# Kernel optimization log

Measured on AMD Instinct MI355X. Metric: run time of the kernel, lower is better.

The kernel has to match this reference:

```python
import jax, jax.numpy as jnp
import numpy as np

HID = 16  # comparator hidden channels, Conv1(2,16) -> Conv1(16,1)


def setup_inputs() -> dict:
    key = jax.random.key(0)
    k0, k1, k2 = jax.random.split(key, 3)
    B, N = 32, 512
    x = jax.random.normal(k0, (B, 1, N), dtype=jnp.float32)
    # xavier_uniform for 1x1 convs, zero bias (as in PermNet.__init__)
    g1 = (6.0 / (2 + HID)) ** 0.5
    g2 = (6.0 / (HID + 1)) ** 0.5
    w1 = jax.random.uniform(k1, (HID, 2), jnp.float32, -g1, g1)
    b1 = jnp.zeros((HID,), jnp.float32)
    w2 = jax.random.uniform(k2, (1, HID), jnp.float32, -g2, g2)
    b2 = jnp.zeros((1,), jnp.float32)
    lr = jnp.ones((1,), jnp.float32)  # learned step size, used via abs()
    return {"x": x, "w1": w1, "b1": b1, "w2": w2, "b2": b2, "lr": lr,
            "steps": 8, "temp": 1}


def reference(x, w1, b1, w2, b2, lr, steps, temp):
    B, C, N = x.shape  # C == 1 (scalar set elements)
    temp = jnp.asarray(temp, x.dtype)

    # --- Comparator: pairwise 1x1-conv MLP over all (i, j) pairs ---
    xi = jnp.broadcast_to(x[:, 0, :, None], (B, N, N))  # element i
    xj = jnp.broadcast_to(x[:, 0, None, :], (B, N, N))  # element j
    pairs = jnp.stack([xi, xj], axis=1)                  # (B, 2, N, N)
    h = jax.nn.relu(jnp.einsum('oc,bcij->boij', w1, pairs)
                    + b1[None, :, None, None])           # (B, HID, N, N)
    c = (jnp.einsum('oc,bcij->boij', w2, h)
         + b2[None, :, None, None])[:, 0]                # (B, N, N)
    c = c - jnp.swapaxes(c, -1, -2)  # antisymmetric ordering cost C(i,j)=-C(j,i)

    # --- calculate_assignment: iterative differentiable permutation ---
    # a[b, i, k] = weight of element i being placed at position k
    lr_abs = jnp.abs(lr)[0]
    a0 = jnp.full((B, N, N), 1.0 / N, dtype=x.dtype)

    def step(a, _):
        csum = jnp.cumsum(a, axis=-1)      # sum_{l<=k} a[., j, l]
        total = csum[..., -1:]
        left = csum - a                     # sum_{l<k}
        right = total - csum                # sum_{l>k}
        m = right - left                    # (B, N, N)
        # d(total cost)/d a_{ik} = sum_j C_{ij} * (right_{jk} - left_{jk})
        grad = jnp.einsum('bij,bjk->bik', c, m)
        a_new = jax.nn.softmax((a - lr_abs * grad) / temp, axis=-1)
        return a_new, None

    a, _ = jax.lax.scan(step, a0, None, length=steps)

    # --- apply_assignment: permute elements into positions ---
    y = jnp.einsum('bci,bik->bck', x, a)  # (B, 1, N)
    return y, a
```

## Files before the change

kernel.cpp:

```cpp
#include <hip/hip_runtime.h>
#include <hip/hip_bf16.h>
#include <math.h>

#define B_   32
#define N_   512
#define HID_ 16

typedef __attribute__((ext_vector_type(8))) short bf16x8;
typedef __attribute__((ext_vector_type(4))) float f32x4;

union U8 { ushort u[8]; uint4 v; };

__device__ __forceinline__ ushort f2bf(float f) {
    __hip_bfloat16 h = __float2bfloat16(f);
    return *reinterpret_cast<ushort*>(&h);
}
__device__ __forceinline__ float bf2f(ushort u) {
    return __uint_as_float(((unsigned int)u) << 16);
}

__device__ __forceinline__ void gload16(const void* g, void* l) {
    __builtin_amdgcn_global_load_lds(
        (const __attribute__((address_space(1))) unsigned int*)g,
        (__attribute__((address_space(3))) unsigned int*)l,
        16, 0, 0);
}

__device__ __forceinline__ int pidx(int r, int c) {
    return r * N_ + ((c + ((r >> 3) << 2)) & (N_ - 1));
}

__global__ __launch_bounds__(512)
void fused_kernel(const float* __restrict__ x,
                  const float* __restrict__ w1,
                  const float* __restrict__ b1,
                  const float* __restrict__ w2,
                  ushort* __restrict__ cB,
                  const ushort* __restrict__ aTin,
                  const ushort* __restrict__ aBin,
                  ushort* __restrict__ aTout,
                  ushort* __restrict__ aBout,
                  float* __restrict__ aout,
                  float* __restrict__ vg,
                  float* __restrict__ ypart,
                  const float* __restrict__ lr,
                  const int* __restrict__ temp,
                  int first, int last)
{
    __shared__ char smem[131072];
    __shared__ float sw1[2*HID_], sb1v[HID_], sw2v[HID_];
    float* Pl = (float*)smem;

    int iblk = blockIdx.x;
    int r8 = iblk & 7, m = iblk >> 3;
    int b  = r8 + ((m >> 3) << 3);
    int i0 = (m & 7) * 64;

    const size_t MATOFF = (size_t)b * N_ * N_;
    int tid = threadIdx.x, lane = tid & 63, w = tid >> 6;

    float lrv = fabsf(lr[0]);
    float ti  = 1.0f / (float)temp[0];
    float vrq[8];

    if (first) {
        if (tid < 2*HID_) sw1[tid] = w1[tid];
        if (tid < HID_)   { sb1v[tid] = b1[tid]; sw2v[tid] = w2[tid]; }
        __syncthreads();
        int k0 = lane * 8;
        float4 xj0 = *(const float4*)&x[b*N_ + k0];
        float4 xj1 = *(const float4*)&x[b*N_ + k0 + 4];
        float xjv[8] = {xj0.x, xj0.y, xj0.z, xj0.w, xj1.x, xj1.y, xj1.z, xj1.w};
        for (int q = 0; q < 8; ++q) {
            int grow = i0 + w*8 + q;
            float xi = x[b*N_ + grow];
            float s1[8] = {}, s2[8] = {};
            for (int o = 0; o < HID_; ++o) {
                float wa = sw1[2*o], wb = sw1[2*o+1], bo = sb1v[o], wo = sw2v[o];
                float Ao = fmaf(wa, xi, bo);
                float Co = fmaf(wb, xi, bo);
#pragma unroll
                for (int e = 0; e < 8; ++e) {
                    s1[e] = fmaf(wo, fmaxf(fmaf(wb, xjv[e], Ao), 0.f), s1[e]);
                    s2[e] = fmaf(wo, fmaxf(fmaf(wa, xjv[e], Co), 0.f), s2[e]);
                }
            }
            float rs = 0.f;
            U8 cb;
#pragma unroll
            for (int e = 0; e < 8; ++e) {
                float cv = s1[e] - s2[e];
                rs += cv;
                cb.u[e] = f2bf(cv);
            }
            *(uint4*)&cB[MATOFF + (size_t)grow * N_ + k0] = cb.v;
#pragma unroll
            for (int off = 1; off < 64; off <<= 1) rs += __shfl_xor(rs, off);
            vrq[q] = rs;
            if (lane == 0) vg[b*N_ + grow] = rs;
        }
    } else {
        const ushort* Ag = cB   + MATOFF + (size_t)i0 * N_;
        const ushort* Bg = aTin + MATOFF + (size_t)(w * 64) * N_;
        char* Asb = smem;
        char* Bw  = smem + 65536 + w * 8192;
        f32x4 acc[4][4] = {};

        {
            int r = tid >> 3, sl = tid & 7;
            const ushort* Asrc = Ag + (size_t)r * N_ + ((sl ^ (r & 7)) << 3);
#pragma unroll
            for (int c = 0; c < 8; ++c)
                gload16(Asrc + c*64, Asb + c*8192 + tid*16);
        }
        asm volatile("s_waitcnt vmcnt(0)" ::: "memory");
        __syncthreads();

        for (int kt = 0; kt < 8; ++kt) {
            asm volatile("s_waitcnt lgkmcnt(0)" ::: "memory");
#pragma unroll
            for (int g = 0; g < 8; ++g) {
                int r  = g*8 + (lane >> 3);
                int sl = lane & 7;
                gload16(Bg + (size_t)r * N_ + kt*64 + ((sl ^ (r & 7)) << 3),
                        Bw + g*1024 + lane*16);
            }
            asm volatile("s_waitcnt vmcnt(0)" ::: "memory");
            __builtin_amdgcn_sched_barrier(0);

#pragma unroll
            for (int kk = 0; kk < 2; ++kk) {
                bf16x8 af[4], bb[4];
#pragma unroll
                for (int f = 0; f < 4; ++f) {
                    int ra = f*16 + (lane & 15);
                    int sa = kk*4 + (lane >> 4);
                    af[f] = *(const bf16x8*)(Asb + kt*8192 + ra*128 + ((sa ^ (ra & 7)) << 4));
                    bb[f] = *(const bf16x8*)(Bw + ra*128 + ((sa ^ (ra & 7)) << 4));
                }
#pragma unroll
                for (int i = 0; i < 4; ++i)
#pragma unroll
                    for (int j = 0; j < 4; ++j)
                        acc[i][j] = __builtin_amdgcn_mfma_f32_16x16x32_bf16(
                                        af[i], bb[j], acc[i][j], 0, 0, 0);
            }
        }
        __syncthreads();

        {
            int h = lane >> 4, cl = lane & 15;
#pragma unroll
            for (int i = 0; i < 4; ++i)
#pragma unroll
                for (int j = 0; j < 4; ++j)
#pragma unroll
                    for (int r = 0; r < 4; ++r)
                        Pl[pidx(i*16 + h*4 + r, w*64 + j*16 + cl)] = acc[i][j][r];
        }
        __syncthreads();
    }

    float ysum[8] = {};

    for (int q = 0; q < 8; ++q) {
        int row  = w*8 + q;
        int grow = i0 + row;
        float vr = first ? vrq[q] : vg[b*N_ + grow];

        float pv[8], av[8];
        if (first) {
#pragma unroll
            for (int e = 0; e < 8; ++e) { pv[e] = vr * (1.0f/N_); av[e] = 1.0f/N_; }
        } else {
            int rot = (row >> 3) << 2;
            int c0  = (lane*8     + rot) & (N_-1);
            int c1  = (lane*8 + 4 + rot) & (N_-1);
            f32x4 p0 = *(const f32x4*)&Pl[row*N_ + c0];
            f32x4 p1 = *(const f32x4*)&Pl[row*N_ + c1];
            pv[0]=p0[0]; pv[1]=p0[1]; pv[2]=p0[2]; pv[3]=p0[3];
            pv[4]=p1[0]; pv[5]=p1[1]; pv[6]=p1[2]; pv[7]=p1[3];
            U8 ab;
            ab.v = *(const uint4*)&aBin[MATOFF + (size_t)grow * N_ + lane*8];
#pragma unroll
            for (int e = 0; e < 8; ++e) av[e] = bf2f(ab.u[e]);
        }

        float cs[8], run = 0.f;
#pragma unroll
        for (int e = 0; e < 8; ++e) { run += pv[e]; cs[e] = run; }
        float laneTot = run;
        float sc = laneTot;
#pragma unroll
        for (int off = 1; off < 64; off <<= 1) {
            float t = __shfl_up(sc, off);
            if (lane >= off) sc += t;
        }
        float excl = sc - laneTot;

        float l[8];
#pragma unroll
        for (int e = 0; e < 8; ++e) {
            float Q    = excl + cs[e];
            float grad = vr - 2.f*Q + pv[e];
            l[e] = (av[e] - lrv*grad) * ti;
        }

        float mx = l[0];
#pragma unroll
        for (int e = 1; e < 8; ++e) mx = fmaxf(mx, l[e]);
#pragma unroll
        for (int off = 1; off < 64; off <<= 1) mx = fmaxf(mx, __shfl_xor(mx, off));

        float ex[8], s = 0.f;
#pragma unroll
        for (int e = 0; e < 8; ++e) { ex[e] = __expf(l[e] - mx); s += ex[e]; }
#pragma unroll
        for (int off = 1; off < 64; off <<= 1) s += __shfl_xor(s, off);

        float inv = 1.0f / s;
#pragma unroll
        for (int e = 0; e < 8; ++e) ex[e] *= inv;

        size_t gbase = MATOFF + (size_t)grow * N_ + lane*8;
        if (last) {
            *(float4*)&aout[gbase]     = make_float4(ex[0], ex[1], ex[2], ex[3]);
            *(float4*)&aout[gbase + 4] = make_float4(ex[4], ex[5], ex[6], ex[7]);
            float xr = x[b*N_ + grow];
#pragma unroll
            for (int e = 0; e < 8; ++e) ysum[e] = fmaf(xr, ex[e], ysum[e]);
        } else {
            U8 ob;
#pragma unroll
            for (int e = 0; e < 8; ++e) ob.u[e] = f2bf(ex[e]);
            *(uint4*)&aBout[gbase] = ob.v;
            int rot = (row >> 3) << 2;
            int c0  = (lane*8     + rot) & (N_-1);
            int c1  = (lane*8 + 4 + rot) & (N_-1);
            *(f32x4*)&Pl[row*N_ + c0] = f32x4{ex[0], ex[1], ex[2], ex[3]};
            *(f32x4*)&Pl[row*N_ + c1] = f32x4{ex[4], ex[5], ex[6], ex[7]};
        }
    }

    if (!last) {
        __syncthreads();
#pragma unroll
        for (int p = 0; p < 8; ++p) {
            int k   = p*64 + (tid >> 3);
            int ii0 = (tid & 7) * 8;
            U8 ob;
#pragma unroll
            for (int e = 0; e < 8; ++e) ob.u[e] = f2bf(Pl[pidx(ii0 + e, k)]);
            *(uint4*)&aTout[MATOFF + (size_t)k * N_ + i0 + ii0] = ob.v;
        }
    } else {
        __syncthreads();
        float* yred = (float*)smem;
        *(f32x4*)&yred[w*512 + lane*8]     = f32x4{ysum[0], ysum[1], ysum[2], ysum[3]};
        *(f32x4*)&yred[w*512 + lane*8 + 4] = f32x4{ysum[4], ysum[5], ysum[6], ysum[7]};
        __syncthreads();
        float acc2 = 0.f;
#pragma unroll
        for (int wv = 0; wv < 8; ++wv) acc2 += yred[wv*512 + tid];
        ypart[(size_t)(b*8 + (i0 >> 6)) * 512 + tid] = acc2;
    }
}

__global__ __launch_bounds__(512)
void y_reduce_kernel(const float* __restrict__ ypart, float* __restrict__ y)
{
    int b = blockIdx.x, k = threadIdx.x;
    float acc = 0.f;
#pragma unroll
    for (int t = 0; t < 8; ++t)
        acc += ypart[(size_t)(b*8 + t) * 512 + k];
    y[b*N_ + k] = acc;
}

extern "C" void kernel_launch(void* const* d_in, const int* in_sizes, int n_in,
                              void* d_out, int out_size, void* d_ws, size_t ws_size,
                              hipStream_t stream)
{
    const float* x  = (const float*)d_in[0];
    const float* w1 = (const float*)d_in[1];
    const float* b1 = (const float*)d_in[2];
    const float* w2 = (const float*)d_in[3];
    const float* lr   = (const float*)d_in[5];
    const int*   temp = (const int*)d_in[7];

    float* y = (float*)d_out;
    float* a = y + B_ * N_;

    const size_t MAT = (size_t)B_ * N_ * N_;
    ushort* cB    = (ushort*)d_ws;
    ushort* aT0   = cB  + MAT;
    ushort* aT1   = aT0 + MAT;
    ushort* aB0   = aT1 + MAT;
    ushort* aB1   = aB0 + MAT;
    float*  v     = (float*)(aB1 + MAT);
    float*  ypart = v + B_ * N_;

    hipLaunchKernelGGL(fused_kernel, dim3(256), dim3(512), 0, stream,
                       x, w1, b1, w2, cB, aT1, aB1, aT0, aB0, a, v, ypart,
                       lr, temp, 1, 0);
    int cur = 0;
    for (int s = 1; s < 7; ++s) {
        ushort* tin  = cur ? aT1 : aT0;
        ushort* binp = cur ? aB1 : aB0;
        ushort* tout = cur ? aT0 : aT1;
        ushort* bout = cur ? aB0 : aB1;
        hipLaunchKernelGGL(fused_kernel, dim3(256), dim3(512), 0, stream,
                           x, w1, b1, w2, cB, tin, binp, tout, bout, a, v, ypart,
                           lr, temp, 0, 0);
        cur ^= 1;
    }
    {
        ushort* tin  = cur ? aT1 : aT0;
        ushort* binp = cur ? aB1 : aB0;
        hipLaunchKernelGGL(fused_kernel, dim3(256), dim3(512), 0, stream,
                           x, w1, b1, w2, cB, tin, binp, aT0, aB0, a, v, ypart,
                           lr, temp, 0, 1);
    }
    hipLaunchKernelGGL(y_reduce_kernel, dim3(B_), dim3(512), 0, stream, ypart, y);
}
```

Measured before the change: 223.8 us.

## Split comparator into separate wide init kernel and prefetch a-rows early

Moves the pairwise comparator MLP out of the first fused_kernel launch into its own init_kernel with 8192 blocks, so that compute is spread over many more threads than the 256-block fused launch gave it. In the later fused steps, the bf16 a-row loads are issued together with the A-tile LDS loads before the wait, hiding their latency behind the GEMM. The row loop is also unrolled by two. The cost is one extra kernel launch and more registers held live for the prefetched rows.

Result: slower. 250.7 us (+12.0%).

```diff
diff --git a/kernel.cpp b/kernel.cpp
--- a/kernel.cpp
+++ b/kernel.cpp
@@ -10,6 +10,7 @@
 typedef __attribute__((ext_vector_type(4))) float f32x4;
 
 union U8 { ushort u[8]; uint4 v; };
+union U4 { ushort u[4]; uint2 v; };
 
 __device__ __forceinline__ ushort f2bf(float f) {
     __hip_bfloat16 h = __float2bfloat16(f);
@@ -30,25 +31,74 @@
     return r * N_ + ((c + ((r >> 3) << 2)) & (N_ - 1));
 }
 
+__global__ __launch_bounds__(256)
+void init_kernel(const float* __restrict__ x,
+                 const float* __restrict__ w1,
+                 const float* __restrict__ b1,
+                 const float* __restrict__ w2,
+                 ushort* __restrict__ cB,
+                 float* __restrict__ v)
+{
+    __shared__ float sw1[2*HID_], sb1[HID_], sw2[HID_];
+    __shared__ float red[4];
+    int tid = threadIdx.x;
+    if (tid < 2*HID_) sw1[tid] = w1[tid];
+    if (tid < HID_)   { sb1[tid] = b1[tid]; sw2[tid] = w2[tid]; }
+    __syncthreads();
+
+    int rowg = blockIdx.x * 2 + (tid >> 7);
+    int b    = rowg >> 9;
+    int col  = (tid & 127) * 4;
+    float xi = x[rowg];
+    float4 xj = *(const float4*)&x[b*N_ + col];
+    float xjv[4] = {xj.x, xj.y, xj.z, xj.w};
+
+    float s1[4] = {}, s2[4] = {};
+#pragma unroll
+    for (int o = 0; o < HID_; ++o) {
+        float wa = sw1[2*o], wb = sw1[2*o+1], bo = sb1[o], wo = sw2[o];
+        float Ao = fmaf(wa, xi, bo);
+        float Co = fmaf(wb, xi, bo);
+#pragma unroll
+        for (int e = 0; e < 4; ++e) {
+            s1[e] = fmaf(wo, fmaxf(fmaf(wb, xjv[e], Ao), 0.f), s1[e]);
+            s2[e] = fmaf(wo, fmaxf(fmaf(wa, xjv[e], Co), 0.f), s2[e]);
+        }
+    }
+
+    float rs = 0.f;
+    U4 cb;
+#pragma unroll
+    for (int e = 0; e < 4; ++e) {
+        float cv = s1[e] - s2[e];
+        rs += cv;
+        cb.u[e] = f2bf(cv);
+    }
+    *(uint2*)&cB[(size_t)rowg * N_ + col] = cb.v;
+
+#pragma unroll
+    for (int off = 1; off < 64; off <<= 1) rs += __shfl_xor(rs, off);
+    int w = tid >> 6;
+    if ((tid & 63) == 0) red[w] = rs;
+    __syncthreads();
+    if (tid < 2) v[blockIdx.x * 2 + tid] = red[2*tid] + red[2*tid + 1];
+}
+
 __global__ __launch_bounds__(512)
 void fused_kernel(const float* __restrict__ x,
-                  const float* __restrict__ w1,
-                  const float* __restrict__ b1,
-                  const float* __restrict__ w2,
-                  ushort* __restrict__ cB,
+                  const ushort* __restrict__ cB,
                   const ushort* __restrict__ aTin,
                   const ushort* __restrict__ aBin,
                   ushort* __restrict__ aTout,
                   ushort* __restrict__ aBout,
                   float* __restrict__ aout,
-                  float* __restrict__ vg,
+                  const float* __restrict__ vg,
                   float* __restrict__ ypart,
                   const float* __restrict__ lr,
                   const int* __restrict__ temp,
                   int first, int last)
 {
     __shared__ char smem[131072];
-    __shared__ float sw1[2*HID_], sb1v[HID_], sw2v[HID_];
     float* Pl = (float*)smem;
 
     int iblk = blockIdx.x;
@@ -61,45 +111,9 @@
 
     float lrv = fabsf(lr[0]);
     float ti  = 1.0f / (float)temp[0];
-    float vrq[8];
-
-    if (first) {
-        if (tid < 2*HID_) sw1[tid] = w1[tid];
-        if (tid < HID_)   { sb1v[tid] = b1[tid]; sw2v[tid] = w2[tid]; }
-        __syncthreads();
-        int k0 = lane * 8;
-        float4 xj0 = *(const float4*)&x[b*N_ + k0];
-        float4 xj1 = *(const float4*)&x[b*N_ + k0 + 4];
-        float xjv[8] = {xj0.x, xj0.y, xj0.z, xj0.w, xj1.x, xj1.y, xj1.z, xj1.w};
-        for (int q = 0; q < 8; ++q) {
-            int grow = i0 + w*8 + q;
-            float xi = x[b*N_ + grow];
-            float s1[8] = {}, s2[8] = {};
-            for (int o = 0; o < HID_; ++o) {
-                float wa = sw1[2*o], wb = sw1[2*o+1], bo = sb1v[o], wo = sw2v[o];
-                float Ao = fmaf(wa, xi, bo);
-                float Co = fmaf(wb, xi, bo);
-#pragma unroll
-                for (int e = 0; e < 8; ++e) {
-                    s1[e] = fmaf(wo, fmaxf(fmaf(wb, xjv[e], Ao), 0.f), s1[e]);
-                    s2[e] = fmaf(wo, fmaxf(fmaf(wa, xjv[e], Co), 0.f), s2[e]);
-                }
-            }
-            float rs = 0.f;
-            U8 cb;
-#pragma unroll
-            for (int e = 0; e < 8; ++e) {
-                float cv = s1[e] - s2[e];
-                rs += cv;
-                cb.u[e] = f2bf(cv);
-            }
-            *(uint4*)&cB[MATOFF + (size_t)grow * N_ + k0] = cb.v;
-#pragma unroll
-            for (int off = 1; off < 64; off <<= 1) rs += __shfl_xor(rs, off);
-            vrq[q] = rs;
-            if (lane == 0) vg[b*N_ + grow] = rs;
-        }
-    } else {
+    uint4 avv[8];
+
+    if (!first) {
         const ushort* Ag = cB   + MATOFF + (size_t)i0 * N_;
         const ushort* Bg = aTin + MATOFF + (size_t)(w * 64) * N_;
         char* Asb = smem;
@@ -113,6 +127,9 @@
             for (int c = 0; c < 8; ++c)
                 gload16(Asrc + c*64, Asb + c*8192 + tid*16);
         }
+#pragma unroll
+        for (int q = 0; q < 8; ++q)
+            avv[q] = *(const uint4*)&aBin[MATOFF + (size_t)(i0 + w*8 + q) * N_ + lane*8];
         asm volatile("s_waitcnt vmcnt(0)" ::: "memory");
         __syncthreads();
 
@@ -163,10 +180,11 @@
 
     float ysum[8] = {};
 
+#pragma unroll 2
     for (int q = 0; q < 8; ++q) {
         int row  = w*8 + q;
         int grow = i0 + row;
-        float vr = first ? vrq[q] : vg[b*N_ + grow];
+        float vr = vg[b*N_ + grow];
 
         float pv[8], av[8];
         if (first) {
@@ -180,8 +198,7 @@
             f32x4 p1 = *(const f32x4*)&Pl[row*N_ + c1];
             pv[0]=p0[0]; pv[1]=p0[1]; pv[2]=p0[2]; pv[3]=p0[3];
             pv[4]=p1[0]; pv[5]=p1[1]; pv[6]=p1[2]; pv[7]=p1[3];
-            U8 ab;
-            ab.v = *(const uint4*)&aBin[MATOFF + (size_t)grow * N_ + lane*8];
+            U8 ab; ab.v = avv[q];
 #pragma unroll
             for (int e = 0; e < 8; ++e) av[e] = bf2f(ab.u[e]);
         }
@@ -300,9 +317,10 @@
     float*  v     = (float*)(aB1 + MAT);
     float*  ypart = v + B_ * N_;
 
+    hipLaunchKernelGGL(init_kernel, dim3(B_*N_/2), dim3(256), 0, stream,
+                       x, w1, b1, w2, cB, v);
     hipLaunchKernelGGL(fused_kernel, dim3(256), dim3(512), 0, stream,
-                       x, w1, b1, w2, cB, aT1, aB1, aT0, aB0, a, v, ypart,
-                       lr, temp, 1, 0);
+                       x, cB, aT1, aB1, aT0, aB0, a, v, ypart, lr, temp, 1, 0);
     int cur = 0;
     for (int s = 1; s < 7; ++s) {
         ushort* tin  = cur ? aT1 : aT0;
@@ -310,7 +328,7 @@
         ushort* tout = cur ? aT0 : aT1;
         ushort* bout = cur ? aB0 : aB1;
         hipLaunchKernelGGL(fused_kernel, dim3(256), dim3(512), 0, stream,
-                           x, w1, b1, w2, cB, tin, binp, tout, bout, a, v, ypart,
+                           x, cB, tin, binp, tout, bout, a, v, ypart,
                            lr, temp, 0, 0);
         cur ^= 1;
     }
@@ -318,7 +336,7 @@
         ushort* tin  = cur ? aT1 : aT0;
         ushort* binp = cur ? aB1 : aB0;
         hipLaunchKernelGGL(fused_kernel, dim3(256), dim3(512), 0, stream,
-                           x, w1, b1, w2, cB, tin, binp, aT0, aB0, a, v, ypart,
+                           x, cB, tin, binp, aT0, aB0, a, v, ypart,
                            lr, temp, 0, 1);
     }
     hipLaunchKernelGGL(y_reduce_kernel, dim3(B_), dim3(512), 0, stream, ypart, y);
```
